# Performance work log

Measured on AMD Instinct MI355X. Metric: run time of the kernel, lower is better.

## Reference

```python
import jax, jax.numpy as jnp
import numpy as np

T, H, I, E, K = 4096, 1024, 2048, 32, 4


def setup_inputs() -> dict:
    key = jax.random.key(0)
    ks = jax.random.split(key, 8)
    s = lambda k, shape, std: (jax.random.normal(k, shape, jnp.float32) * std)
    return {
        "x": s(ks[0], (T, H), 1.0),
        "router_w": s(ks[1], (E, H), 0.02),
        "gate_w": s(ks[2], (E, H, I), 0.02),
        "up_w": s(ks[3], (E, H, I), 0.02),
        "down_w": s(ks[4], (E, I, H), 0.02),
        "shared_gate_w": s(ks[5], (H, I), 0.02),
        "shared_up_w": s(ks[6], (H, I), 0.02),
        "shared_down_w": s(ks[7], (I, H), 0.02),
        "top_k": K,
    }


def _moe_forward(x, router_w, gate_w, up_w, down_w, sg, su, sd, top_k):
    # x: [T, H]; expert weights: gate/up [E, H, I], down [E, I, H]
    Tn = x.shape[0]
    En = router_w.shape[0]

    # Router: softmax over experts, top-k selection, renormalize selected probs
    logits = x @ router_w.T                                   # [T, E]
    probs = jax.nn.softmax(logits, axis=-1)
    topk_p, topk_i = jax.lax.top_k(probs, top_k)              # [T, K]
    topk_p = topk_p / jnp.sum(topk_p, axis=-1, keepdims=True)

    # Dense combine weights: combine[t, e] = routing weight of expert e for token t
    combine = jnp.zeros((Tn, En), x.dtype).at[
        jnp.arange(Tn)[:, None], topk_i].add(topk_p)          # [T, E]

    def expert_step(acc, inp):
        wg, wu, wd, c = inp                                   # [H,I], [H,I], [I,H], [T]
        h = jax.nn.silu(x @ wg) * (x @ wu)                    # [T, I] SwiGLU
        return acc + c[:, None] * (h @ wd), None

    acc0 = jnp.zeros_like(x)
    out, _ = jax.lax.scan(expert_step, acc0,
                          (gate_w, up_w, down_w, combine.T))

    # Shared expert: always applied
    shared = (jax.nn.silu(x @ sg) * (x @ su)) @ sd            # [T, H]
    return out + shared


def reference(x, router_w, gate_w, up_w, down_w,
              shared_gate_w, shared_up_w, shared_down_w, top_k):
    return _moe_forward(x, router_w, gate_w, up_w, down_w,
                        shared_gate_w, shared_up_w, shared_down_w, top_k)
```

## Files before the change

kernel.cpp:

```cpp
#include <hip/hip_runtime.h>
#include <hip/hip_bf16.h>

#define T_TOK 4096
#define H_DIM 1024
#define I_DIM 2048
#define N_EXP 32
#define TOPK  4
#define TKTOT (T_TOK * TOPK)
#define ROWS_MAX 24576
#define MAX_TILES 192
#define BM 128
#define BK 64
#define LDB 72

typedef _Float16 f16;
typedef __attribute__((ext_vector_type(2))) f16  f16x2;
typedef __attribute__((ext_vector_type(4))) f16  f16x4;
typedef __attribute__((ext_vector_type(8))) f16  f16x8;
typedef __attribute__((ext_vector_type(4))) float f32x4;

__global__ void prep_kernel(const float* __restrict__ x, f16* __restrict__ xb,
                            int* __restrict__ row_token,
                            float* __restrict__ row_weight,
                            int* __restrict__ counts) {
  int gid = blockIdx.x * blockDim.x + threadIdx.x;
  float4 v = *(const float4*)(x + (size_t)gid * 4);
  f16x4 hv = { (f16)v.x, (f16)v.y, (f16)v.z, (f16)v.w };
  *(f16x4*)(xb + (size_t)gid * 4) = hv;
  if (gid < ROWS_MAX) {
    row_token[gid]  = (gid < T_TOK) ? gid : 0;
    row_weight[gid] = (gid < T_TOK) ? 1.f : 0.f;
  }
  if (gid < N_EXP) counts[gid] = 0;
}

__global__ void router_kernel(const float* __restrict__ x,
                              const float* __restrict__ rw,
                              int* __restrict__ expert_sel,
                              float* __restrict__ weight_sel,
                              int* __restrict__ counts) {
  int wid = threadIdx.x >> 6, lane = threadIdx.x & 63;
  int t = blockIdx.x * 4 + wid;
  float xr[16];
#pragma unroll
  for (int j = 0; j < 16; ++j) xr[j] = x[(size_t)t * H_DIM + lane + j * 64];
  float l[32];
#pragma unroll
  for (int e = 0; e < 32; ++e) {
    float p = 0.f;
#pragma unroll
    for (int j = 0; j < 16; ++j) p += xr[j] * rw[(size_t)e * H_DIM + lane + j * 64];
#pragma unroll
    for (int off = 32; off; off >>= 1) p += __shfl_xor(p, off, 64);
    l[e] = p;
  }
  if (lane == 0) {
    unsigned used = 0;
    int sel[4]; float lv[4];
#pragma unroll
    for (int k = 0; k < 4; ++k) {
      float bv = -3.4e38f; int bi = 0;
#pragma unroll
      for (int e = 0; e < 32; ++e) {
        bool better = (((used >> e) & 1u) == 0u) && (l[e] > bv);
        bv = better ? l[e] : bv;
        bi = better ? e : bi;
      }
      used |= 1u << bi; sel[k] = bi; lv[k] = bv;
    }
    float m = lv[0];
    float p0 = __expf(lv[0] - m), p1 = __expf(lv[1] - m);
    float p2 = __expf(lv[2] - m), p3 = __expf(lv[3] - m);
    float s = p0 + p1 + p2 + p3;
    float wv[4] = { p0 / s, p1 / s, p2 / s, p3 / s };
#pragma unroll
    for (int k = 0; k < 4; ++k) {
      expert_sel[t * 4 + k] = sel[k];
      weight_sel[t * 4 + k] = wv[k];
      atomicAdd(&counts[sel[k]], 1);
    }
  }
}

__global__ void scan_kernel(const int* __restrict__ counts, int* __restrict__ cursor,
                            int* __restrict__ tile_expert, int* __restrict__ tile_row0,
                            int* __restrict__ ntiles) {
  if (threadIdx.x != 0 || blockIdx.x != 0) return;
  int nt = 0;
  for (int i = 0; i < T_TOK / BM; ++i) { tile_expert[nt] = N_EXP; tile_row0[nt] = i * BM; ++nt; }
  int pos = T_TOK;
  for (int e = 0; e < N_EXP; ++e) {
    cursor[e] = pos;
    int c = counts[e];
    int nte = (c + BM - 1) / BM;
    for (int i = 0; i < nte; ++i) { tile_expert[nt] = e; tile_row0[nt] = pos + i * BM; ++nt; }
    pos += nte * BM;
  }
  ntiles[0] = nt;
}

__global__ void scatter_kernel(const int* __restrict__ expert_sel,
                               const float* __restrict__ weight_sel,
                               int* __restrict__ cursor,
                               int* __restrict__ row_token,
                               float* __restrict__ row_weight) {
  int i = blockIdx.x * blockDim.x + threadIdx.x;
  if (i >= TKTOT) return;
  int e = expert_sel[i];
  int pos = atomicAdd(&cursor[e], 1);
  row_token[pos]  = i >> 2;
  row_weight[pos] = weight_sel[i];
}

struct Bf2 { float2 g[8]; };
__device__ __forceinline__ Bf2 fetch_b2(const float* __restrict__ src, size_t ldn) {
  Bf2 r;
#pragma unroll
  for (int j = 0; j < 8; ++j) r.g[j] = *(const float2*)(src + (size_t)j * ldn);
  return r;
}
__device__ __forceinline__ void write_b2(const Bf2& b,
                                         f16 (*__restrict__ Bs)[LDB], int nq, int kr) {
  const float* ga = (const float*)b.g;
  int ks = (8 * kr) ^ ((nq & 7) << 3);
#pragma unroll
  for (int i = 0; i < 2; ++i) {
    union { f16x2 p[4]; f16x8 v; } u;
#pragma unroll
    for (int j = 0; j < 4; ++j)
      u.p[j] = __builtin_bit_cast(
          f16x2, __builtin_amdgcn_cvt_pkrtz(ga[(2 * j) * 2 + i],
                                            ga[(2 * j + 1) * 2 + i]));
    *(f16x8*)&Bs[2 * nq + i][ks] = u.v;
  }
}
__device__ __forceinline__ int rswz1(int row, int kf16) {
  return kf16 ^ (((row >> 1) & 7) << 3);
}

struct Bf4 { float4 g[8]; };
__device__ __forceinline__ Bf4 fetch_b4(const float* __restrict__ src, size_t ldn) {
  Bf4 r;
#pragma unroll
  for (int j = 0; j < 8; ++j) r.g[j] = *(const float4*)(src + (size_t)j * ldn);
  return r;
}
__device__ __forceinline__ void write_b4(const Bf4& b,
                                         f16 (*__restrict__ Bs)[LDB], int nq, int kr) {
  const float* ga = (const float*)b.g;
  int ks = (8 * kr) ^ ((nq & 7) << 3);
#pragma unroll
  for (int i = 0; i < 4; ++i) {
    union { f16x2 p[4]; f16x8 v; } u;
#pragma unroll
    for (int j = 0; j < 4; ++j)
      u.p[j] = __builtin_bit_cast(
          f16x2, __builtin_amdgcn_cvt_pkrtz(ga[(2 * j) * 4 + i],
                                            ga[(2 * j + 1) * 4 + i]));
    *(f16x8*)&Bs[4 * nq + i][ks] = u.v;
  }
}
__device__ __forceinline__ int rswz2(int row, int kf16) {
  return kf16 ^ (((row >> 2) & 7) << 3);
}

__global__ __launch_bounds__(256, 3) void gemm1_kernel(
    const f16* __restrict__ xb,
    const float* __restrict__ gate_w, const float* __restrict__ up_w,
    const float* __restrict__ sgw, const float* __restrict__ suw,
    const int* __restrict__ row_token,
    const int* __restrict__ tile_expert, const int* __restrict__ tile_row0,
    const int* __restrict__ ntiles, f16* __restrict__ hbuf) {
  int d = blockIdx.y * gridDim.x + blockIdx.x;
  int l = (d & 7) * 768 + (d >> 3);
  int bx = l % MAX_TILES;
  int n0 = (l / MAX_TILES) * 64;
  if (bx >= ntiles[0]) return;
  int e = tile_expert[bx];
  int row0 = tile_row0[bx];
  const float* wg = (e < N_EXP) ? gate_w + (size_t)e * H_DIM * I_DIM : sgw;
  const float* wu = (e < N_EXP) ? up_w   + (size_t)e * H_DIM * I_DIM : suw;

  __shared__ __align__(16) f16 smem[BM * LDB + 2 * 64 * LDB];
  f16 (*As)[LDB] = (f16(*)[LDB])smem;
  f16 (*Bg)[LDB] = (f16(*)[LDB])(smem + BM * LDB);
  f16 (*Bu)[LDB] = (f16(*)[LDB])(smem + BM * LDB + 64 * LDB);
  f16 (*Ct)[LDB] = (f16(*)[LDB])smem;

  int tid = threadIdx.x;
  int lane = tid & 63, wid = tid >> 6;
  int wm = wid >> 1, wn = wid & 1;
  int lr = lane & 15, lk = (lane >> 4) * 8;
  int nq = tid & 31, kr = tid >> 5;

  int atok[4];
#pragma unroll
  for (int it = 0; it < 4; ++it)
    atok[it] = row_token[row0 + ((tid + it * 256) >> 3)];

  const float* wgp = wg + (size_t)(8 * kr) * I_DIM + n0 + 2 * nq;
  const float* wup = wu + (size_t)(8 * kr) * I_DIM + n0 + 2 * nq;

  f32x4 accg[4][2], accu[4][2];
#pragma unroll
  for (int m = 0; m < 4; ++m)
#pragma unroll
    for (int n = 0; n < 2; ++n) { accg[m][n] = (f32x4)0.f; accu[m][n] = (f32x4)0.f; }

  f16x8 pa[4];
#pragma unroll
  for (int it = 0; it < 4; ++it) {
    int idx = tid + it * 256;
    pa[it] = *(const f16x8*)(xb + (size_t)atok[it] * H_DIM + (idx & 7) * 8);
  }
  Bf2 pg = fetch_b2(wgp, I_DIM);
  Bf2 pu = fetch_b2(wup, I_DIM);

  for (int ks = 0; ks < H_DIM / BK; ++ks) {
#pragma unroll
    for (int it = 0; it < 4; ++it) {
      int idx = tid + it * 256;
      *(f16x8*)&As[idx >> 3][(idx & 7) * 8] = pa[it];
    }
    write_b2(pg, Bg, nq, kr);
    write_b2(pu, Bu, nq, kr);
    if (ks + 1 < H_DIM / BK) {
      int k0n = (ks + 1) * BK;
#pragma unroll
      for (int it = 0; it < 4; ++it) {
        int idx = tid + it * 256;
        pa[it] = *(const f16x8*)(xb + (size_t)atok[it] * H_DIM + k0n + (idx & 7) * 8);
      }
      pg = fetch_b2(wgp + (size_t)k0n * I_DIM, I_DIM);
      pu = fetch_b2(wup + (size_t)k0n * I_DIM, I_DIM);
    }
    __syncthreads();
#pragma unroll
    for (int kk = 0; kk < BK; kk += 32) {
      f16x8 a[4], bg[2], bu[2];
#pragma unroll
      for (int m = 0; m < 4; ++m)
        a[m] = *(const f16x8*)&As[wm * 64 + m * 16 + lr][kk + lk];
#pragma unroll
      for (int n = 0; n < 2; ++n) {
        int rowb = wn * 32 + n * 16 + lr;
        int ko = rswz1(rowb, kk + lk);
        bg[n] = *(const f16x8*)&Bg[rowb][ko];
        bu[n] = *(const f16x8*)&Bu[rowb][ko];
      }
#pragma unroll
      for (int m = 0; m < 4; ++m)
#pragma unroll
        for (int n = 0; n < 2; ++n) {
          accg[m][n] = __builtin_amdgcn_mfma_f32_16x16x32_f16(a[m], bg[n], accg[m][n], 0, 0, 0);
          accu[m][n] = __builtin_amdgcn_mfma_f32_16x16x32_f16(a[m], bu[n], accu[m][n], 0, 0, 0);
        }
    }
    __syncthreads();
  }
#pragma unroll
  for (int m = 0; m < 4; ++m)
#pragma unroll
    for (int n = 0; n < 2; ++n)
#pragma unroll
      for (int j = 0; j < 4; ++j) {
        float g = accg[m][n][j], u = accu[m][n][j];
        float hv = g / (1.f + __expf(-g)) * u;
        Ct[wm * 64 + m * 16 + (lane >> 4) * 4 + j][wn * 32 + n * 16 + lr] = (f16)hv;
      }
  __syncthreads();
#pragma unroll
  for (int it = 0; it < 4; ++it) {
    int idx = tid + it * 256;
    int r = idx >> 3, g8 = (idx & 7) * 8;
    *(f16x8*)(hbuf + (size_t)(row0 + r) * I_DIM + n0 + g8) = *(const f16x8*)&Ct[r][g8];
  }
}

__global__ __launch_bounds__(256, 3) void gemm2_kernel(
    const f16* __restrict__ hbuf,
    const float* __restrict__ down_w, const float* __restrict__ sdw,
    const int* __restrict__ row_token, const float* __restrict__ row_weight,
    const int* __restrict__ tile_expert, const int* __restrict__ tile_row0,
    const int* __restrict__ ntiles, float* __restrict__ out) {
  int d = blockIdx.y * gridDim.x + blockIdx.x;
  int l = (d & 7) * 192 + (d >> 3);
  int bx = l % MAX_TILES;
  int n0 = (l / MAX_TILES) * 128;
  if (bx >= ntiles[0]) return;
  int e = tile_expert[bx];
  int row0 = tile_row0[bx];
  const float* wd = (e < N_EXP) ? down_w + (size_t)e * I_DIM * H_DIM : sdw;

  __shared__ __align__(16) f16 smem[2 * BM * LDB];
  f16 (*As)[LDB] = (f16(*)[LDB])smem;
  f16 (*Bd)[LDB] = (f16(*)[LDB])(smem + BM * LDB);

  int tid = threadIdx.x;
  int lane = tid & 63, wid = tid >> 6;
  int wm = wid >> 1, wn = wid & 1;
  int lr = lane & 15, lk = (lane >> 4) * 8;
  int nq = tid & 31, kr = tid >> 5;

  const float* wdp = wd + (size_t)(8 * kr) * H_DIM + n0 + 4 * nq;

  f32x4 acc[4][4];
#pragma unroll
  for (int m = 0; m < 4; ++m)
#pragma unroll
    for (int n = 0; n < 4; ++n) acc[m][n] = (f32x4)0.f;

  f16x8 pa[4];
#pragma unroll
  for (int it = 0; it < 4; ++it) {
    int idx = tid + it * 256;
    pa[it] = *(const f16x8*)(hbuf + (size_t)(row0 + (idx >> 3)) * I_DIM + (idx & 7) * 8);
  }
  Bf4 pd = fetch_b4(wdp, H_DIM);

  for (int ks = 0; ks < I_DIM / BK; ++ks) {
#pragma unroll
    for (int it = 0; it < 4; ++it) {
      int idx = tid + it * 256;
      *(f16x8*)&As[idx >> 3][(idx & 7) * 8] = pa[it];
    }
    write_b4(pd, Bd, nq, kr);
    if (ks + 1 < I_DIM / BK) {
      int k0n = (ks + 1) * BK;
#pragma unroll
      for (int it = 0; it < 4; ++it) {
        int idx = tid + it * 256;
        pa[it] = *(const f16x8*)(hbuf + (size_t)(row0 + (idx >> 3)) * I_DIM + k0n + (idx & 7) * 8);
      }
      pd = fetch_b4(wdp + (size_t)k0n * H_DIM, H_DIM);
    }
    __syncthreads();
#pragma unroll
    for (int kk = 0; kk < BK; kk += 32) {
      f16x8 a[4], bd[4];
#pragma unroll
      for (int m = 0; m < 4; ++m)
        a[m] = *(const f16x8*)&As[wm * 64 + m * 16 + lr][kk + lk];
#pragma unroll
      for (int n = 0; n < 4; ++n) {
        int rowb = wn * 64 + n * 16 + lr;
        bd[n] = *(const f16x8*)&Bd[rowb][rswz2(rowb, kk + lk)];
      }
#pragma unroll
      for (int m = 0; m < 4; ++m)
#pragma unroll
        for (int n = 0; n < 4; ++n)
          acc[m][n] = __builtin_amdgcn_mfma_f32_16x16x32_f16(a[m], bd[n], acc[m][n], 0, 0, 0);
    }
    __syncthreads();
  }
#pragma unroll
  for (int m = 0; m < 4; ++m)
#pragma unroll
    for (int j = 0; j < 4; ++j) {
      int rr = row0 + wm * 64 + m * 16 + (lane >> 4) * 4 + j;
      int tok = row_token[rr];
      float wgt = row_weight[rr];
      if (wgt != 0.f) {
        float* op = out + (size_t)tok * H_DIM + n0 + wn * 64 + lr;
#pragma unroll
        for (int n = 0; n < 4; ++n) atomicAdd(op + n * 16, wgt * acc[m][n][j]);
      }
    }
}

extern "C" void kernel_launch(void* const* d_in, const int* in_sizes, int n_in,
                              void* d_out, int out_size, void* d_ws, size_t ws_size,
                              hipStream_t stream) {
  const float* x        = (const float*)d_in[0];
  const float* router_w = (const float*)d_in[1];
  const float* gate_w   = (const float*)d_in[2];
  const float* up_w     = (const float*)d_in[3];
  const float* down_w   = (const float*)d_in[4];
  const float* sgw      = (const float*)d_in[5];
  const float* suw      = (const float*)d_in[6];
  const float* sdw      = (const float*)d_in[7];
  float* out = (float*)d_out;

  char* w = (char*)d_ws;
  f16*   xb         = (f16*)w;   w += (size_t)T_TOK * H_DIM * 2;
  int*   expert_sel = (int*)w;   w += (size_t)TKTOT * 4;
  float* weight_sel = (float*)w; w += (size_t)TKTOT * 4;
  int*   counts     = (int*)w;   w += 256;
  int*   cursor     = (int*)w;   w += 256;
  int*   tile_exp   = (int*)w;   w += MAX_TILES * 4;
  int*   tile_row0  = (int*)w;   w += MAX_TILES * 4;
  int*   ntiles     = (int*)w;   w += 256;
  int*   row_token  = (int*)w;   w += (size_t)ROWS_MAX * 4;
  float* row_weight = (float*)w; w += (size_t)ROWS_MAX * 4;
  f16*   hbuf       = (f16*)w;   w += (size_t)ROWS_MAX * I_DIM * 2;
  if ((size_t)(w - (char*)d_ws) > ws_size) return;

  (void)hipMemsetAsync(d_out, 0, (size_t)out_size * sizeof(float), stream);
  prep_kernel<<<(T_TOK * H_DIM / 4) / 256, 256, 0, stream>>>(x, xb, row_token, row_weight, counts);
  router_kernel<<<T_TOK / 4, 256, 0, stream>>>(x, router_w, expert_sel, weight_sel, counts);
  scan_kernel<<<1, 64, 0, stream>>>(counts, cursor, tile_exp, tile_row0, ntiles);
  scatter_kernel<<<TKTOT / 256, 256, 0, stream>>>(expert_sel, weight_sel, cursor, row_token, row_weight);
  gemm1_kernel<<<dim3(MAX_TILES, I_DIM / 64), 256, 0, stream>>>(
      xb, gate_w, up_w, sgw, suw, row_token, tile_exp, tile_row0, ntiles, hbuf);
  gemm2_kernel<<<dim3(MAX_TILES, H_DIM / 128), 256, 0, stream>>>(
      hbuf, down_w, sdw, row_token, row_weight, tile_exp, tile_row0, ntiles, out);
}
```

Measured before the change: 669.5 us.

## Use async global-to-LDS A loads and replace atomic combine with gather kernel

The A operand in both grouped GEMMs is now loaded with global_load_lds directly into double-buffered, XOR-swizzled shared memory instead of going through registers. gemm2 shrinks its N tile to 64, writes per-row f16 results to a staging buffer, and a new gather kernel sums the shared expert and the four routed expert rows per token using the stored slot indices and weights. This removes the float atomicAdd scatter into the output and the output memset. In exchange it adds an extra f16 intermediate buffer with its write and re-read, rounds expert outputs to f16 before combining, and doubles the gemm2 grid.

```diff
diff --git a/kernel.cpp b/kernel.cpp
--- a/kernel.cpp
+++ b/kernel.cpp
@@ -19,18 +19,20 @@
 typedef __attribute__((ext_vector_type(8))) f16  f16x8;
 typedef __attribute__((ext_vector_type(4))) float f32x4;
 
+__device__ __forceinline__ void glds16(const f16* g, f16* l) {
+  __builtin_amdgcn_global_load_lds(
+      (const __attribute__((address_space(1))) void*)g,
+      (__attribute__((address_space(3))) void*)l, 16, 0, 0);
+}
+
 __global__ void prep_kernel(const float* __restrict__ x, f16* __restrict__ xb,
                             int* __restrict__ row_token,
-                            float* __restrict__ row_weight,
                             int* __restrict__ counts) {
   int gid = blockIdx.x * blockDim.x + threadIdx.x;
   float4 v = *(const float4*)(x + (size_t)gid * 4);
   f16x4 hv = { (f16)v.x, (f16)v.y, (f16)v.z, (f16)v.w };
   *(f16x4*)(xb + (size_t)gid * 4) = hv;
-  if (gid < ROWS_MAX) {
-    row_token[gid]  = (gid < T_TOK) ? gid : 0;
-    row_weight[gid] = (gid < T_TOK) ? 1.f : 0.f;
-  }
+  if (gid < ROWS_MAX) row_token[gid] = (gid < T_TOK) ? gid : 0;
   if (gid < N_EXP) counts[gid] = 0;
 }
 
@@ -103,13 +105,14 @@
                                const float* __restrict__ weight_sel,
                                int* __restrict__ cursor,
                                int* __restrict__ row_token,
-                               float* __restrict__ row_weight) {
+                               int* __restrict__ slot_of) {
   int i = blockIdx.x * blockDim.x + threadIdx.x;
   if (i >= TKTOT) return;
   int e = expert_sel[i];
   int pos = atomicAdd(&cursor[e], 1);
-  row_token[pos]  = i >> 2;
-  row_weight[pos] = weight_sel[i];
+  row_token[pos] = i >> 2;
+  slot_of[i] = pos;
+  (void)weight_sel;
 }
 
 struct Bf2 { float2 g[8]; };
@@ -136,32 +139,6 @@
 }
 __device__ __forceinline__ int rswz1(int row, int kf16) {
   return kf16 ^ (((row >> 1) & 7) << 3);
-}
-
-struct Bf4 { float4 g[8]; };
-__device__ __forceinline__ Bf4 fetch_b4(const float* __restrict__ src, size_t ldn) {
-  Bf4 r;
-#pragma unroll
-  for (int j = 0; j < 8; ++j) r.g[j] = *(const float4*)(src + (size_t)j * ldn);
-  return r;
-}
-__device__ __forceinline__ void write_b4(const Bf4& b,
-                                         f16 (*__restrict__ Bs)[LDB], int nq, int kr) {
-  const float* ga = (const float*)b.g;
-  int ks = (8 * kr) ^ ((nq & 7) << 3);
-#pragma unroll
-  for (int i = 0; i < 4; ++i) {
-    union { f16x2 p[4]; f16x8 v; } u;
-#pragma unroll
-    for (int j = 0; j < 4; ++j)
-      u.p[j] = __builtin_bit_cast(
-          f16x2, __builtin_amdgcn_cvt_pkrtz(ga[(2 * j) * 4 + i],
-                                            ga[(2 * j + 1) * 4 + i]));
-    *(f16x8*)&Bs[4 * nq + i][ks] = u.v;
-  }
-}
-__device__ __forceinline__ int rswz2(int row, int kf16) {
-  return kf16 ^ (((row >> 2) & 7) << 3);
 }
 
 __global__ __launch_bounds__(256, 3) void gemm1_kernel(
@@ -181,10 +158,11 @@
   const float* wg = (e < N_EXP) ? gate_w + (size_t)e * H_DIM * I_DIM : sgw;
   const float* wu = (e < N_EXP) ? up_w   + (size_t)e * H_DIM * I_DIM : suw;
 
-  __shared__ __align__(16) f16 smem[BM * LDB + 2 * 64 * LDB];
-  f16 (*As)[LDB] = (f16(*)[LDB])smem;
-  f16 (*Bg)[LDB] = (f16(*)[LDB])(smem + BM * LDB);
-  f16 (*Bu)[LDB] = (f16(*)[LDB])(smem + BM * LDB + 64 * LDB);
+  __shared__ __align__(16) f16 smem[2 * BM * BK + 2 * 64 * LDB];
+  f16* A0 = smem;
+  f16* A1 = smem + BM * BK;
+  f16 (*Bg)[LDB] = (f16(*)[LDB])(smem + 2 * BM * BK);
+  f16 (*Bu)[LDB] = (f16(*)[LDB])(smem + 2 * BM * BK + 64 * LDB);
   f16 (*Ct)[LDB] = (f16(*)[LDB])smem;
 
   int tid = threadIdx.x;
@@ -193,11 +171,14 @@
   int lr = lane & 15, lk = (lane >> 4) * 8;
   int nq = tid & 31, kr = tid >> 5;
 
-  int atok[4];
-#pragma unroll
-  for (int it = 0; it < 4; ++it)
-    atok[it] = row_token[row0 + ((tid + it * 256) >> 3)];
-
+  const f16* abase[4];
+#pragma unroll
+  for (int it = 0; it < 4; ++it) {
+    int idx = tid + it * 256;
+    int arow = idx >> 3;
+    int atok = row_token[row0 + arow];
+    abase[it] = xb + (size_t)atok * H_DIM + ((((idx & 7)) ^ (arow & 7)) << 3);
+  }
   const float* wgp = wg + (size_t)(8 * kr) * I_DIM + n0 + 2 * nq;
   const float* wup = wu + (size_t)(8 * kr) * I_DIM + n0 + 2 * nq;
 
@@ -207,40 +188,35 @@
 #pragma unroll
     for (int n = 0; n < 2; ++n) { accg[m][n] = (f32x4)0.f; accu[m][n] = (f32x4)0.f; }
 
-  f16x8 pa[4];
-#pragma unroll
-  for (int it = 0; it < 4; ++it) {
-    int idx = tid + it * 256;
-    pa[it] = *(const f16x8*)(xb + (size_t)atok[it] * H_DIM + (idx & 7) * 8);
-  }
+#pragma unroll
+  for (int it = 0; it < 4; ++it)
+    glds16(abase[it], A0 + (tid + it * 256) * 8);
   Bf2 pg = fetch_b2(wgp, I_DIM);
   Bf2 pu = fetch_b2(wup, I_DIM);
 
   for (int ks = 0; ks < H_DIM / BK; ++ks) {
-#pragma unroll
-    for (int it = 0; it < 4; ++it) {
-      int idx = tid + it * 256;
-      *(f16x8*)&As[idx >> 3][(idx & 7) * 8] = pa[it];
-    }
     write_b2(pg, Bg, nq, kr);
     write_b2(pu, Bu, nq, kr);
     if (ks + 1 < H_DIM / BK) {
       int k0n = (ks + 1) * BK;
-#pragma unroll
-      for (int it = 0; it < 4; ++it) {
-        int idx = tid + it * 256;
-        pa[it] = *(const f16x8*)(xb + (size_t)atok[it] * H_DIM + k0n + (idx & 7) * 8);
-      }
+      f16* ad = ((ks + 1) & 1) ? A1 : A0;
+#pragma unroll
+      for (int it = 0; it < 4; ++it)
+        glds16(abase[it] + k0n, ad + (tid + it * 256) * 8);
       pg = fetch_b2(wgp + (size_t)k0n * I_DIM, I_DIM);
       pu = fetch_b2(wup + (size_t)k0n * I_DIM, I_DIM);
     }
     __syncthreads();
+    const f16* As = (ks & 1) ? A1 : A0;
 #pragma unroll
     for (int kk = 0; kk < BK; kk += 32) {
       f16x8 a[4], bg[2], bu[2];
 #pragma unroll
-      for (int m = 0; m < 4; ++m)
-        a[m] = *(const f16x8*)&As[wm * 64 + m * 16 + lr][kk + lk];
+      for (int m = 0; m < 4; ++m) {
+        int ar = wm * 64 + m * 16 + lr;
+        int ko = (kk + lk) ^ ((ar & 7) << 3);
+        a[m] = *(const f16x8*)(As + ar * BK + ko);
+      }
 #pragma unroll
       for (int n = 0; n < 2; ++n) {
         int rowb = wn * 32 + n * 16 + lr;
@@ -280,21 +256,22 @@
 __global__ __launch_bounds__(256, 3) void gemm2_kernel(
     const f16* __restrict__ hbuf,
     const float* __restrict__ down_w, const float* __restrict__ sdw,
-    const int* __restrict__ row_token, const float* __restrict__ row_weight,
     const int* __restrict__ tile_expert, const int* __restrict__ tile_row0,
-    const int* __restrict__ ntiles, float* __restrict__ out) {
+    const int* __restrict__ ntiles, f16* __restrict__ ybuf) {
   int d = blockIdx.y * gridDim.x + blockIdx.x;
-  int l = (d & 7) * 192 + (d >> 3);
+  int l = (d & 7) * 384 + (d >> 3);
   int bx = l % MAX_TILES;
-  int n0 = (l / MAX_TILES) * 128;
+  int n0 = (l / MAX_TILES) * 64;
   if (bx >= ntiles[0]) return;
   int e = tile_expert[bx];
   int row0 = tile_row0[bx];
   const float* wd = (e < N_EXP) ? down_w + (size_t)e * I_DIM * H_DIM : sdw;
 
-  __shared__ __align__(16) f16 smem[2 * BM * LDB];
-  f16 (*As)[LDB] = (f16(*)[LDB])smem;
-  f16 (*Bd)[LDB] = (f16(*)[LDB])(smem + BM * LDB);
+  __shared__ __align__(16) f16 smem[2 * BM * BK + 64 * LDB];
+  f16* A0 = smem;
+  f16* A1 = smem + BM * BK;
+  f16 (*Bd)[LDB] = (f16(*)[LDB])(smem + 2 * BM * BK);
+  f16 (*Ct)[LDB] = (f16(*)[LDB])smem;
 
   int tid = threadIdx.x;
   int lane = tid & 63, wid = tid >> 6;
@@ -302,54 +279,56 @@
   int lr = lane & 15, lk = (lane >> 4) * 8;
   int nq = tid & 31, kr = tid >> 5;
 
-  const float* wdp = wd + (size_t)(8 * kr) * H_DIM + n0 + 4 * nq;
-
-  f32x4 acc[4][4];
-#pragma unroll
-  for (int m = 0; m < 4; ++m)
-#pragma unroll
-    for (int n = 0; n < 4; ++n) acc[m][n] = (f32x4)0.f;
-
-  f16x8 pa[4];
+  const f16* abase[4];
 #pragma unroll
   for (int it = 0; it < 4; ++it) {
     int idx = tid + it * 256;
-    pa[it] = *(const f16x8*)(hbuf + (size_t)(row0 + (idx >> 3)) * I_DIM + (idx & 7) * 8);
-  }
-  Bf4 pd = fetch_b4(wdp, H_DIM);
+    int arow = idx >> 3;
+    abase[it] = hbuf + (size_t)(row0 + arow) * I_DIM + ((((idx & 7)) ^ (arow & 7)) << 3);
+  }
+  const float* wdp = wd + (size_t)(8 * kr) * H_DIM + n0 + 2 * nq;
+
+  f32x4 acc[4][2];
+#pragma unroll
+  for (int m = 0; m < 4; ++m)
+#pragma unroll
+    for (int n = 0; n < 2; ++n) acc[m][n] = (f32x4)0.f;
+
+#pragma unroll
+  for (int it = 0; it < 4; ++it)
+    glds16(abase[it], A0 + (tid + it * 256) * 8);
+  Bf2 pd = fetch_b2(wdp, H_DIM);
 
   for (int ks = 0; ks < I_DIM / BK; ++ks) {
-#pragma unroll
-    for (int it = 0; it < 4; ++it) {
-      int idx = tid + it * 256;
-      *(f16x8*)&As[idx >> 3][(idx & 7) * 8] = pa[it];
-    }
-    write_b4(pd, Bd, nq, kr);
+    write_b2(pd, Bd, nq, kr);
     if (ks + 1 < I_DIM / BK) {
       int k0n = (ks + 1) * BK;
-#pragma unroll
-      for (int it = 0; it < 4; ++it) {
-        int idx = tid + it * 256;
-        pa[it] = *(const f16x8*)(hbuf + (size_t)(row0 + (idx >> 3)) * I_DIM + k0n + (idx & 7) * 8);
-      }
-      pd = fetch_b4(wdp + (size_t)k0n * H_DIM, H_DIM);
+      f16* ad = ((ks + 1) & 1) ? A1 : A0;
+#pragma unroll
+      for (int it = 0; it < 4; ++it)
+        glds16(abase[it] + k0n, ad + (tid + it * 256) * 8);
+      pd = fetch_b2(wdp + (size_t)k0n * H_DIM, H_DIM);
     }
     __syncthreads();
+    const f16* As = (ks & 1) ? A1 : A0;
 #pragma unroll
     for (int kk = 0; kk < BK; kk += 32) {
-      f16x8 a[4], bd[4];
+      f16x8 a[4], bd[2];
+#pragma unroll
+      for (int m = 0; m < 4; ++m) {
+        int ar = wm * 64 + m * 16 + lr;
+        int ko = (kk + lk) ^ ((ar & 7) << 3);
+        a[m] = *(const f16x8*)(As + ar * BK + ko);
+      }
+#pragma unroll
+      for (int n = 0; n < 2; ++n) {
+        int rowb = wn * 32 + n * 16 + lr;
+        bd[n] = *(const f16x8*)&Bd[rowb][rswz1(rowb, kk + lk)];
+      }
 #pragma unroll
       for (int m = 0; m < 4; ++m)
-        a[m] = *(const f16x8*)&As[wm * 64 + m * 16 + lr][kk + lk];
-#pragma unroll
-      for (int n = 0; n < 4; ++n) {
-        int rowb = wn * 64 + n * 16 + lr;
-        bd[n] = *(const f16x8*)&Bd[rowb][rswz2(rowb, kk + lk)];
-      }
-#pragma unroll
-      for (int m = 0; m < 4; ++m)
-#pragma unroll
-        for (int n = 0; n < 4; ++n)
+#pragma unroll
+        for (int n = 0; n < 2; ++n)
           acc[m][n] = __builtin_amdgcn_mfma_f32_16x16x32_f16(a[m], bd[n], acc[m][n], 0, 0, 0);
     }
     __syncthreads();
@@ -357,16 +336,42 @@
 #pragma unroll
   for (int m = 0; m < 4; ++m)
 #pragma unroll
-    for (int j = 0; j < 4; ++j) {
-      int rr = row0 + wm * 64 + m * 16 + (lane >> 4) * 4 + j;
-      int tok = row_token[rr];
-      float wgt = row_weight[rr];
-      if (wgt != 0.f) {
-        float* op = out + (size_t)tok * H_DIM + n0 + wn * 64 + lr;
-#pragma unroll
-        for (int n = 0; n < 4; ++n) atomicAdd(op + n * 16, wgt * acc[m][n][j]);
-      }
-    }
+    for (int n = 0; n < 2; ++n)
+#pragma unroll
+      for (int j = 0; j < 4; ++j)
+        Ct[wm * 64 + m * 16 + (lane >> 4) * 4 + j][wn * 32 + n * 16 + lr] =
+            (f16)acc[m][n][j];
+  __syncthreads();
+#pragma unroll
+  for (int it = 0; it < 4; ++it) {
+    int idx = tid + it * 256;
+    int r = idx >> 3, g8 = (idx & 7) * 8;
+    *(f16x8*)(ybuf + (size_t)(row0 + r) * H_DIM + n0 + g8) = *(const f16x8*)&Ct[r][g8];
+  }
+}
+
+__global__ void gather_kernel(const f16* __restrict__ ybuf,
+                              const int* __restrict__ slot_of,
+                              const float* __restrict__ weight_sel,
+                              float* __restrict__ out) {
+  int gid = blockIdx.x * blockDim.x + threadIdx.x;
+  int t = gid >> 7, s8 = (gid & 127) * 8;
+  f16x8 ysh = *(const f16x8*)(ybuf + (size_t)t * H_DIM + s8);
+  float a[8];
+#pragma unroll
+  for (int j = 0; j < 8; ++j) a[j] = (float)ysh[j];
+#pragma unroll
+  for (int k = 0; k < 4; ++k) {
+    int sl = slot_of[t * 4 + k];
+    float w = weight_sel[t * 4 + k];
+    f16x8 v = *(const f16x8*)(ybuf + (size_t)sl * H_DIM + s8);
+#pragma unroll
+    for (int j = 0; j < 8; ++j) a[j] += w * (float)v[j];
+  }
+  float4 o0 = { a[0], a[1], a[2], a[3] };
+  float4 o1 = { a[4], a[5], a[6], a[7] };
+  *(float4*)(out + (size_t)t * H_DIM + s8) = o0;
+  *(float4*)(out + (size_t)t * H_DIM + s8 + 4) = o1;
 }
 
 extern "C" void kernel_launch(void* const* d_in, const int* in_sizes, int n_in,
@@ -386,23 +391,25 @@
   f16*   xb         = (f16*)w;   w += (size_t)T_TOK * H_DIM * 2;
   int*   expert_sel = (int*)w;   w += (size_t)TKTOT * 4;
   float* weight_sel = (float*)w; w += (size_t)TKTOT * 4;
+  int*   slot_of    = (int*)w;   w += (size_t)TKTOT * 4;
   int*   counts     = (int*)w;   w += 256;
   int*   cursor     = (int*)w;   w += 256;
   int*   tile_exp   = (int*)w;   w += MAX_TILES * 4;
   int*   tile_row0  = (int*)w;   w += MAX_TILES * 4;
   int*   ntiles     = (int*)w;   w += 256;
   int*   row_token  = (int*)w;   w += (size_t)ROWS_MAX * 4;
-  float* row_weight = (float*)w; w += (size_t)ROWS_MAX * 4;
   f16*   hbuf       = (f16*)w;   w += (size_t)ROWS_MAX * I_DIM * 2;
+  f16*   ybuf       = (f16*)w;   w += (size_t)ROWS_MAX * H_DIM * 2;
   if ((size_t)(w - (char*)d_ws) > ws_size) return;
 
-  (void)hipMemsetAsync(d_out, 0, (size_t)out_size * sizeof(float), stream);
-  prep_kernel<<<(T_TOK * H_DIM / 4) / 256, 256, 0, stream>>>(x, xb, row_token, row_weight, counts);
+  prep_kernel<<<(T_TOK * H_DIM / 4) / 256, 256, 0, stream>>>(x, xb, row_token, counts);
   router_kernel<<<T_TOK / 4, 256, 0, stream>>>(x, router_w, expert_sel, weight_sel, counts);
   scan_kernel<<<1, 64, 0, stream>>>(counts, cursor, tile_exp, tile_row0, ntiles);
-  scatter_kernel<<<TKTOT / 256, 256, 0, stream>>>(expert_sel, weight_sel, cursor, row_token, row_weight);
+  scatter_kernel<<<TKTOT / 256, 256, 0, stream>>>(expert_sel, weight_sel, cursor, row_token, slot_of);
   gemm1_kernel<<<dim3(MAX_TILES, I_DIM / 64), 256, 0, stream>>>(
       xb, gate_w, up_w, sgw, suw, row_token, tile_exp, tile_row0, ntiles, hbuf);
-  gemm2_kernel<<<dim3(MAX_TILES, H_DIM / 128), 256, 0, stream>>>(
-      hbuf, down_w, sdw, row_token, row_weight, tile_exp, tile_row0, ntiles, out);
-}
+  gemm2_kernel<<<dim3(MAX_TILES, H_DIM / 64), 256, 0, stream>>>(
+      hbuf, down_w, sdw, tile_exp, tile_row0, ntiles, ybuf);
+  gather_kernel<<<(T_TOK * (H_DIM / 8)) / 256, 256, 0, stream>>>(
+      ybuf, slot_of, weight_sel, out);
+}
```

After: 745.6 us. 11.4% more time.
